# Performance work log

Measured on AMD Instinct MI355X. Metric: run time of the kernel, lower is better.

The kernel has to match this reference:

```python
import jax, jax.numpy as jnp
import numpy as np

NUM_HEADS = 8
HEAD_DIM = 64
HIDDEN_SIZE = 128
TOP_K = 16
EPS = 1e-6


def setup_inputs() -> dict:
    key = jax.random.key(0)
    k1, k2, k3 = jax.random.split(key, 3)
    B, H, S, D = 4, NUM_HEADS, 1024, HEAD_DIM
    return {
        "keys": jax.random.normal(k1, (B, H, S, D), dtype=jnp.float32),
        "values": jax.random.normal(k2, (B, H, S, D), dtype=jnp.float32),
        "queries": jax.random.normal(k3, (B, H, S, D), dtype=jnp.float32),
    }


def _project(x):
    # replicate [B,H,S,D] along last dim to cover HIDDEN_SIZE basis indices
    D = x.shape[-1]
    if D >= HIDDEN_SIZE:
        return x[..., :HIDDEN_SIZE]
    repeats = (HIDDEN_SIZE + D - 1) // D
    return jnp.tile(x, (1, 1, 1, repeats))[..., :HIDDEN_SIZE]


def reference(keys, values, queries):
    B, H, S, D = keys.shape
    b_idx = jnp.arange(B)[:, None, None]   # [B,1,1]
    h_idx = jnp.arange(H)[None, :, None]   # [1,H,1]

    # ---- update: scatter-add outer products into assigned memory bank ----
    assignments = jnp.argmax(jnp.abs(_project(keys)), axis=-1)  # [B,H,S]
    outer = values[..., :, None] * keys[..., None, :]           # [B,H,S,D,D] (v k^T)
    M = jnp.zeros((B, H, HIDDEN_SIZE, D, D), dtype=keys.dtype)
    M = M.at[b_idx, h_idx, assignments].add(outer)
    z = jnp.zeros((B, H, HIDDEN_SIZE, D), dtype=keys.dtype)
    z = z.at[b_idx, h_idx, assignments].add(keys)

    # ---- retrieve: top-k basis selection, gather-matvec, weighted combine ----
    scores = jnp.abs(_project(queries))                          # [B,H,S,HIDDEN]
    top_scores, top_idx = jax.lax.top_k(scores, TOP_K)           # [B,H,S,K]
    weights = jax.nn.softmax(top_scores, axis=-1)

    output = jnp.zeros((B, H, S, D), dtype=queries.dtype)
    for k in range(TOP_K):
        mem = top_idx[..., k]                                    # [B,H,S]
        M_sel = M[b_idx, h_idx, mem]                             # [B,H,S,D,D]
        z_sel = z[b_idx, h_idx, mem]                             # [B,H,S,D]
        num = jnp.einsum('bhsde,bhse->bhsd', M_sel, queries)
        den = jnp.einsum('bhsd,bhsd->bhs', z_sel, queries)[..., None] + EPS
        output = output + weights[..., k:k + 1] * (num / den)
    return output
```

## Files before the change

kernel.cpp:

```cpp
#include <hip/hip_runtime.h>
#include <math.h>

#define S_LEN 1024
#define EPS 1e-6f

typedef __attribute__((ext_vector_type(8)))  short bf16x8;
typedef __attribute__((ext_vector_type(4)))  short bf16x4;
typedef __attribute__((ext_vector_type(16))) float float16v;


__device__ __forceinline__ void bar_lgkm() {
    asm volatile("s_waitcnt lgkmcnt(0)" ::: "memory");
    __builtin_amdgcn_s_barrier();
    __builtin_amdgcn_sched_barrier(0);
    asm volatile("" ::: "memory");
}

__device__ __forceinline__ unsigned short f2bf(float f) {
    unsigned int u = __float_as_uint(f);
    unsigned int r = (u + 0x7fffu + ((u >> 16) & 1u)) >> 16;
    return (unsigned short)r;
}

__device__ __forceinline__ bf16x8 pack8(float4 a, float4 b) {
    bf16x8 r;
    r[0] = (short)f2bf(a.x); r[1] = (short)f2bf(a.y);
    r[2] = (short)f2bf(a.z); r[3] = (short)f2bf(a.w);
    r[4] = (short)f2bf(b.x); r[5] = (short)f2bf(b.y);
    r[6] = (short)f2bf(b.z); r[7] = (short)f2bf(b.w);
    return r;
}

__global__ __launch_bounds__(512) void k_pre(const float* __restrict__ keys,
                                             const float* __restrict__ queries,
                                             int* __restrict__ kcnt2,
                                             unsigned short* __restrict__ klist2,
                                             int* __restrict__ qcnt2,
                                             unsigned* __restrict__ qpair,
                                             unsigned char* __restrict__ qflag,
                                             float* __restrict__ out) {
    const int bh   = blockIdx.x >> 5;
    const int blk  = blockIdx.x & 31;
    const int wv   = threadIdx.x >> 6;
    const int lane = threadIdx.x & 63;

    __shared__ int khist[64], qhist[64];
    if (threadIdx.x < 64) { khist[threadIdx.x] = 0; qhist[threadIdx.x] = 0; }
    __syncthreads();

    const int s0 = blk * 32 + wv * 4;
    float kv[4], qv[4];
    #pragma unroll
    for (int i = 0; i < 4; ++i) {
        kv[i] = keys   [((size_t)bh * 1024 + s0 + i) * 64 + lane];
        qv[i] = queries[((size_t)bh * 1024 + s0 + i) * 64 + lane];
    }

    {
        float4 zz = {0.f, 0.f, 0.f, 0.f};
        float4* po = (float4*)(out + (size_t)blockIdx.x * 2048);
        po[threadIdx.x] = zz;
    }

    float bv[4]; int bi[4];
    #pragma unroll
    for (int i = 0; i < 4; ++i) { bv[i] = fabsf(kv[i]); bi[i] = lane; }
    #pragma unroll
    for (int off = 1; off < 64; off <<= 1) {
        #pragma unroll
        for (int i = 0; i < 4; ++i) {
            float ov = __shfl_xor(bv[i], off, 64);
            int   oi = __shfl_xor(bi[i], off, 64);
            if (ov > bv[i] || (ov == bv[i] && oi < bi[i])) { bv[i] = ov; bi[i] = oi; }
        }
    }
    #pragma unroll
    for (int i = 0; i < 4; ++i) {
        if (lane == 0) {
            int pos = atomicAdd(&khist[bi[i]], 1);
            klist2[((size_t)bh * 64 + bi[i]) * 1024 + blk * 32 + pos] =
                (unsigned short)(s0 + i);
        }
    }

    unsigned ud[4]; int gt[4];
    #pragma unroll
    for (int i = 0; i < 4; ++i) {
        ud[i] = __float_as_uint(qv[i]) & 0x7fffffffu;
        gt[i] = 0;
    }
    #pragma unroll
    for (int k = 0; k < 64; ++k) {
        #pragma unroll
        for (int i = 0; i < 4; ++i) {
            unsigned ui = (unsigned)__builtin_amdgcn_readlane((int)ud[i], k);
            gt[i] += (ui > ud[i]) ? 1 : 0;
        }
    }
    int S[4];
    #pragma unroll
    for (int i = 0; i < 4; ++i) S[i] = gt[i];
    #pragma unroll
    for (int off = 1; off < 64; off <<= 1) {
        #pragma unroll
        for (int i = 0; i < 4; ++i) S[i] += __shfl_xor(S[i], off, 64);
    }
    float e[4];
    #pragma unroll
    for (int i = 0; i < 4; ++i) e[i] = expf(__uint_as_float(ud[i]));
    int copies[4], contrib[4], rank[4];
    #pragma unroll
    for (int i = 0; i < 4; ++i) {
        if (S[i] == 2016) {
            contrib[i] = (gt[i] < 8);
            copies[i]  = contrib[i] ? 2 : 0;
            rank[i]    = gt[i];
        } else {
            int eq = 0, eql = 0;
            #pragma unroll
            for (int k = 0; k < 64; ++k) {
                unsigned ui = (unsigned)__builtin_amdgcn_readlane((int)ud[i], k);
                eq  += (ui == ud[i]) ? 1 : 0;
                eql += (ui == ud[i] && k < lane) ? 1 : 0;
            }
            int pos_low  = 2 * gt[i] + eql;
            int pos_high = pos_low + eq;
            copies[i]  = (pos_low < 16 ? 1 : 0) + (pos_high < 16 ? 1 : 0);
            contrib[i] = (pos_low < 16);
            rank[i]    = 15;
        }
    }
    float ce[4];
    #pragma unroll
    for (int i = 0; i < 4; ++i) ce[i] = (float)copies[i] * e[i];
    #pragma unroll
    for (int off = 1; off < 64; off <<= 1) {
        #pragma unroll
        for (int i = 0; i < 4; ++i) ce[i] += __shfl_xor(ce[i], off, 64);
    }
    #pragma unroll
    for (int i = 0; i < 4; ++i) {
        if (contrib[i]) {
            int pos = atomicAdd(&qhist[lane], 1);
            unsigned wb = __float_as_uint(e[i] / ce[i]) & 0xFFFFC000u;
            qpair[((size_t)bh * 64 + lane) * 1024 + blk * 32 + pos] =
                wb | ((unsigned)rank[i] << 10) | (unsigned)(s0 + i);
        }
        if (qflag && lane == 0)
            qflag[bh * 1024 + s0 + i] = (S[i] == 2016) ? 0 : 1;
    }
    __syncthreads();
    if (threadIdx.x < 64) {
        kcnt2[(bh * 32 + blk) * 64 + threadIdx.x] = khist[threadIdx.x];
        qcnt2[(bh * 32 + blk) * 64 + threadIdx.x] = qhist[threadIdx.x];
    }
}

__global__ __launch_bounds__(256) void k_build(const float* __restrict__ keys,
                                               const float* __restrict__ values,
                                               const int* __restrict__ kcnt2,
                                               const unsigned short* __restrict__ klist2,
                                               unsigned short* __restrict__ M_g,
                                               float* __restrict__ z_g,
                                               int* __restrict__ nm_g) {
    const int g    = blockIdx.x;
    const int bh   = g >> 6;
    const int bank = g & 63;
    const int t    = threadIdx.x;
    const int lane = t & 63;
    const int grp  = t >> 6;

    __shared__ float stg[2][1024];
    __shared__ unsigned short s_match[256];
    __shared__ int koffs_s[33];

    if (t < 32) {
        int c = kcnt2[(bh * 32 + t) * 64 + bank];
        #pragma unroll
        for (int off = 1; off < 32; off <<= 1) {
            int o = __shfl(c, t - off, 64);
            if (t >= off) c += o;
        }
        if (t == 0) koffs_s[0] = 0;
        koffs_s[t + 1] = c;
    }
    bar_lgkm();
    const int nm = koffs_s[32];
    if (t == 0) nm_g[g] = nm;
    if (nm == 0) return;

    float acc[16];
    #pragma unroll
    for (int m = 0; m < 16; ++m) acc[m] = 0.f;
    float zacc = 0.f;
    const float* kb = keys   + (size_t)bh * S_LEN * 64;
    const float* vb = values + (size_t)bh * S_LEN * 64;
    int it = 0;
    for (int cb = 0; cb < nm; cb += 256) {
        const int cn = min(256, nm - cb);
        bar_lgkm();
        if (t < cn) {
            int idx = cb + t;
            int seg = 0;
            #pragma unroll
            for (int i = 1; i < 32; ++i) if (idx >= koffs_s[i]) seg = i;
            s_match[t] = klist2[(size_t)(bh * 64 + bank) * 1024 + seg * 32 +
                                (idx - koffs_s[seg])];
        }
        bar_lgkm();
        for (int base = 0; base < cn; base += 8, ++it) {
            float* kst = stg[it & 1];
            float* vst = kst + 512;
            #pragma unroll
            for (int rr = 0; rr < 2; ++rr) {
                int row = grp + rr * 4;
                if (base + row < cn) {
                    int s = s_match[base + row];
                    kst[row * 64 + lane] = kb[(size_t)s * 64 + lane];
                    vst[row * 64 + lane] = vb[(size_t)s * 64 + lane];
                }
            }
            bar_lgkm();
            int lim = min(8, cn - base);
            for (int jj = 0; jj < lim; ++jj) {
                float kv = kst[jj * 64 + lane];
                #pragma unroll
                for (int m = 0; m < 16; ++m)
                    acc[m] += vst[jj * 64 + grp * 16 + m] * kv;
            }
            if (t < 64)
                for (int jj = 0; jj < lim; ++jj) zacc += kst[jj * 64 + t];
        }
    }
    unsigned short* mg = M_g + (size_t)g * 4096;
    #pragma unroll
    for (int m = 0; m < 16; ++m) {
        int dv = grp * 16 + m;
        mg[dv * 64 + (((lane >> 3) ^ (dv & 7)) << 3) + (lane & 7)] = f2bf(acc[m]);
    }
    if (t < 64) z_g[(size_t)g * 64 + t] = zacc;
}

template <bool GM, bool SC>
__global__ __launch_bounds__(256) void k_main_t(const float* __restrict__ keys,
                                                const float* __restrict__ values,
                                                const float* __restrict__ queries,
                                                const int* __restrict__ kcnt2,
                                                const unsigned short* __restrict__ klist2,
                                                const int* __restrict__ qcnt2,
                                                const unsigned* __restrict__ qpair,
                                                const unsigned short* __restrict__ M_g,
                                                const float* __restrict__ z_g,
                                                const int* __restrict__ nm_g,
                                                unsigned short* __restrict__ Obuf,
                                                float* __restrict__ out) {
    const int g     = blockIdx.x;
    const int gb    = g >> 1;
    const int split = g & 1;
    const int bh    = gb >> 6;
    const int bank  = gb & 63;
    const int t     = threadIdx.x;
    const int lane  = t & 63;
    const int grp   = t >> 6;

    __shared__ alignas(16) unsigned short M_bf[64 * 64];
    __shared__ alignas(16) unsigned short Q_bf[64 * 64];
    __shared__ alignas(16) unsigned short Ou_bf[64 * 68];
    __shared__ unsigned short s_match[256];
    __shared__ unsigned q_ent[256];
    __shared__ int    koffs_s[33], qoffs_s[33];
    __shared__ float  z_s[64];
    __shared__ double den_s[64];
    __shared__ float  w_s[2][64];
    __shared__ int    sq_s[2][64];

    if constexpr (GM) {
        if (t < 32) {
            int c = qcnt2[(bh * 32 + t) * 64 + bank];
            #pragma unroll
            for (int off = 1; off < 32; off <<= 1) {
                int o = __shfl(c, t - off, 64);
                if (t >= off) c += o;
            }
            if (t == 0) qoffs_s[0] = 0;
            qoffs_s[t + 1] = c;
        }
    } else {
        if (t < 64) {
            int i = t & 31;
            int c = (t < 32) ? kcnt2[(bh * 32 + i) * 64 + bank]
                             : qcnt2[(bh * 32 + i) * 64 + bank];
            #pragma unroll
            for (int off = 1; off < 32; off <<= 1) {
                int o = __shfl(c, t - off, 64);
                if (i >= off) c += o;
            }
            if (t < 32) { if (i == 0) koffs_s[0] = 0; koffs_s[i + 1] = c; }
            else        { if (i == 0) qoffs_s[0] = 0; qoffs_s[i + 1] = c; }
        }
    }
    bar_lgkm();

    const int nq   = qoffs_s[32];
    const int half = (nq + 1) >> 1;
    const int jlo  = split * half;
    const int jhi  = min(nq, jlo + half);
    int nm;
    if constexpr (GM) nm = nm_g[gb]; else nm = koffs_s[32];
    if (jhi <= jlo) return;
    if (nm == 0) {
        if constexpr (SC) {
            for (int jg = jlo + t; jg < jhi; jg += 256) {
                int seg = 0;
                #pragma unroll
                for (int i = 1; i < 32; ++i) if (jg >= qoffs_s[i]) seg = i;
                unsigned e = qpair[(size_t)(bh * 64 + bank) * 1024 + seg * 32 +
                                   (jg - qoffs_s[seg])];
                int r = (e >> 10) & 15;
                if (r < 8) {
                    uint4 z4 = {0u, 0u, 0u, 0u};
                    uint4* dst = (uint4*)&Obuf[(((size_t)bh * 1024 +
                                 (e & 1023u)) * 8 + r) * 64];
                    #pragma unroll
                    for (int x = 0; x < 8; ++x) dst[x] = z4;
                }
            }
        }
        return;
    }

    if constexpr (GM) {
        const unsigned short* mg = M_g + (size_t)gb * 4096;
        *(bf16x8*)&M_bf[t * 8]        = *(const bf16x8*)&mg[t * 8];
        *(bf16x8*)&M_bf[2048 + t * 8] = *(const bf16x8*)&mg[2048 + t * 8];
        if (t < 64) z_s[t] = z_g[(size_t)gb * 64 + t];
    } else {
        float acc[16];
        #pragma unroll
        for (int m = 0; m < 16; ++m) acc[m] = 0.f;
        float zacc = 0.f;
        const float* kb = keys   + (size_t)bh * S_LEN * 64;
        const float* vb = values + (size_t)bh * S_LEN * 64;
        int it = 0;
        for (int cb = 0; cb < nm; cb += 256) {
            const int cn = min(256, nm - cb);
            bar_lgkm();
            if (t < cn) {
                int idx = cb + t;
                int seg = 0;
                #pragma unroll
                for (int i = 1; i < 32; ++i) if (idx >= koffs_s[i]) seg = i;
                s_match[t] = klist2[(size_t)(bh * 64 + bank) * 1024 + seg * 32 +
                                    (idx - koffs_s[seg])];
            }
            bar_lgkm();
            for (int base = 0; base < cn; base += 8, ++it) {
                float* kst = (float*)Ou_bf + (it & 1) * 1024;
                float* vst = kst + 512;
                #pragma unroll
                for (int rr = 0; rr < 2; ++rr) {
                    int row = grp + rr * 4;
                    if (base + row < cn) {
                        int s = s_match[base + row];
                        kst[row * 64 + lane] = kb[(size_t)s * 64 + lane];
                        vst[row * 64 + lane] = vb[(size_t)s * 64 + lane];
                    }
                }
                bar_lgkm();
                int lim = min(8, cn - base);
                for (int jj = 0; jj < lim; ++jj) {
                    float kv = kst[jj * 64 + lane];
                    #pragma unroll
                    for (int m = 0; m < 16; ++m)
                        acc[m] += vst[jj * 64 + grp * 16 + m] * kv;
                }
                if (t < 64)
                    for (int jj = 0; jj < lim; ++jj) zacc += kst[jj * 64 + t];
            }
        }
        #pragma unroll
        for (int m = 0; m < 16; ++m) {
            int dv = grp * 16 + m;
            M_bf[dv * 64 + (((lane >> 3) ^ (dv & 7)) << 3) + (lane & 7)] = f2bf(acc[m]);
        }
        if (t < 64) z_s[t] = zacc;
    }

    const float* qb = queries + (size_t)bh * S_LEN * 64;
    float*       ob = out     + (size_t)bh * S_LEN * 64;
    unsigned short* obuf_b = SC ? Obuf + (size_t)bh * 1024 * 512 : nullptr;
    const int dvh = grp >> 1, jh = grp & 1;
    const int hi  = lane >> 5;
    const int nqL = jhi - jlo;
    const int jq  = t >> 2, cq = t & 3;

    int prev_nb = 0;
    bool have_pf = false;
    float4 f0, f1, f2, f3;
    unsigned pe = 0;
    for (int qloc = 0, batch = 0; qloc < nqL; qloc += 64, ++batch) {
        const int nb  = min(64, nqL - qloc);
        const int cur = batch & 1;

        if ((qloc & 255) == 0) {
            if (qloc + t < nqL) {
                int jg = jlo + qloc + t;
                int seg = 0;
                #pragma unroll
                for (int i = 1; i < 32; ++i) if (jg >= qoffs_s[i]) seg = i;
                q_ent[t] = qpair[(size_t)(bh * 64 + bank) * 1024 + seg * 32 +
                                 (jg - qoffs_s[seg])];
            }
            bar_lgkm();
        }

        unsigned e = 0;
        const bool act = (jq < nb);
        if (act) {
            e = have_pf ? pe : q_ent[(qloc & 255) + jq];
            if (!have_pf) {
                const float4* src =
                    (const float4*)(qb + (size_t)(e & 1023u) * 64 + cq * 16);
                f0 = src[0]; f1 = src[1]; f2 = src[2]; f3 = src[3];
            }
        }

        if (batch > 0) {
            #pragma unroll
            for (int jj = 0; jj < 16; ++jj) {
                int j = grp * 16 + jj;
                if (j < prev_nb) {
                    unsigned short vb16 = Ou_bf[j * 68 + lane];
                    int sr = sq_s[1 - cur][j];
                    int s  = sr & 1023;
                    if constexpr (SC) {
                        int r = (sr >> 10) & 15;
                        if (r < 8)
                            obuf_b[((size_t)s * 8 + r) * 64 + lane] = vb16;
                        else
                            unsafeAtomicAdd(&ob[(size_t)s * 64 + lane],
                                __uint_as_float((unsigned)vb16 << 16));
                    } else {
                        unsafeAtomicAdd(&ob[(size_t)s * 64 + lane],
                            __uint_as_float((unsigned)vb16 << 16));
                    }
                }
            }
        }

        {
            bf16x8 p0 = {}, p1 = {};
            double d = 0.0;
            if (act) {
                if ((t & 3) == 0) {
                    sq_s[cur][jq] = (int)(e & 0x3FFFu);
                    w_s[cur][jq]  = __uint_as_float(e & 0xFFFFC000u);
                }
                p0 = pack8(f0, f1);
                p1 = pack8(f2, f3);
                const float4* zz4 = (const float4*)&z_s[cq * 16];
                float4 z0 = zz4[0], z1 = zz4[1], z2 = zz4[2], z3 = zz4[3];
                double da, db;
                da  = (double)z0.x * f0.x + (double)z0.y * f0.y + (double)z0.z * f0.z + (double)z0.w * f0.w;
                db  = (double)z1.x * f1.x + (double)z1.y * f1.y + (double)z1.z * f1.z + (double)z1.w * f1.w;
                da += (double)z2.x * f2.x + (double)z2.y * f2.y + (double)z2.z * f2.z + (double)z2.w * f2.w;
                db += (double)z3.x * f3.x + (double)z3.y * f3.y + (double)z3.z * f3.z + (double)z3.w * f3.w;
                d = da + db;
            }
            int c0 = cq * 2;
            *(bf16x8*)&Q_bf[jq * 64 + ((c0 ^ (jq & 7)) << 3)]       = p0;
            *(bf16x8*)&Q_bf[jq * 64 + (((c0 + 1) ^ (jq & 7)) << 3)] = p1;
            d += __shfl_xor(d, 1, 64);
            d += __shfl_xor(d, 2, 64);
            if ((t & 3) == 0) den_s[jq] = d;
        }

        {
            const int qn = qloc + 64;
            have_pf = false;
            if (qn < nqL && (qn & 255) != 0) {
                int nbn = min(64, nqL - qn);
                if (jq < nbn) {
                    pe = q_ent[(qn & 255) + jq];
                    const float4* src =
                        (const float4*)(qb + (size_t)(pe & 1023u) * 64 + cq * 16);
                    f0 = src[0]; f1 = src[1]; f2 = src[2]; f3 = src[3];
                    have_pf = true;
                }
            }
        }
        bar_lgkm();

        float16v C;
        #pragma unroll
        for (int i = 0; i < 16; ++i) C[i] = 0.f;
        const int am = dvh * 32 + (lane & 31);
        const int bn = jh  * 32 + (lane & 31);
        #pragma unroll
        for (int ks = 0; ks < 4; ++ks) {
            int ch = ks * 2 + hi;
            bf16x8 af = *(const bf16x8*)&M_bf[am * 64 + ((ch ^ (am & 7)) << 3)];
            bf16x8 bf = *(const bf16x8*)&Q_bf[bn * 64 + ((ch ^ (bn & 7)) << 3)];
            C = __builtin_amdgcn_mfma_f32_32x32x16_bf16(af, bf, C, 0, 0, 0);
        }
        {
            double den = den_s[bn];
            float  w   = w_s[cur][bn];
            float rinv = (float)((double)w / (den + (double)EPS));
            #pragma unroll
            for (int rq = 0; rq < 4; ++rq) {
                bf16x4 pk;
                pk[0] = (short)f2bf(C[rq * 4 + 0] * rinv);
                pk[1] = (short)f2bf(C[rq * 4 + 1] * rinv);
                pk[2] = (short)f2bf(C[rq * 4 + 2] * rinv);
                pk[3] = (short)f2bf(C[rq * 4 + 3] * rinv);
                *(bf16x4*)&Ou_bf[bn * 68 + dvh * 32 + rq * 8 + hi * 4] = pk;
            }
        }
        bar_lgkm();
        prev_nb = nb;
    }
    {
        const int cur = (((nqL + 63) >> 6) - 1) & 1;
        #pragma unroll
        for (int jj = 0; jj < 16; ++jj) {
            int j = grp * 16 + jj;
            if (j < prev_nb) {
                unsigned short vb16 = Ou_bf[j * 68 + lane];
                int sr = sq_s[cur][j];
                int s  = sr & 1023;
                if constexpr (SC) {
                    int r = (sr >> 10) & 15;
                    if (r < 8)
                        obuf_b[((size_t)s * 8 + r) * 64 + lane] = vb16;
                    else
                        unsafeAtomicAdd(&ob[(size_t)s * 64 + lane],
                            __uint_as_float((unsigned)vb16 << 16));
                } else {
                    unsafeAtomicAdd(&ob[(size_t)s * 64 + lane],
                        __uint_as_float((unsigned)vb16 << 16));
                }
            }
        }
    }
}

__global__ __launch_bounds__(256) void k_reduce(const unsigned short* __restrict__ Obuf,
                                                const unsigned char* __restrict__ qflag,
                                                float* __restrict__ out) {
    const int wv   = threadIdx.x >> 6;
    const int lane = threadIdx.x & 63;
    const int q0   = (blockIdx.x * 4 + wv) * 8;
    #pragma unroll
    for (int i = 0; i < 8; ++i) {
        int q = q0 + i;
        if (qflag[q]) continue;
        const unsigned short* obr = Obuf + (size_t)q * 512;
        float acc = 0.f;
        #pragma unroll
        for (int r = 0; r < 8; ++r)
            acc += __uint_as_float((unsigned)obr[r * 64 + lane] << 16);
        out[(size_t)q * 64 + lane] = acc;
    }
}

extern "C" void kernel_launch(void* const* d_in, const int* in_sizes, int n_in,
                              void* d_out, int out_size, void* d_ws, size_t ws_size,
                              hipStream_t stream) {
    const float* keys    = (const float*)d_in[0];
    const float* values  = (const float*)d_in[1];
    const float* queries = (const float*)d_in[2];
    char* ws = (char*)d_ws;
    int*            kcnt2  = (int*)(ws);
    int*            qcnt2  = (int*)(ws + 262144);
    unsigned short* klist2 = (unsigned short*)(ws + 524288);
    unsigned*       qpair  = (unsigned*)(ws + 4718592);
    unsigned short* M_g    = (unsigned short*)(ws + 13107200);
    float*          z_g    = (float*)(ws + 29884416);
    int*            nm_g   = (int*)(ws + 30408704);
    unsigned char*  qflag  = (unsigned char*)(ws + 30416896);
    unsigned short* Obuf   = (unsigned short*)(ws + 30449664);
    const bool big  = (ws_size >= 30416896u);
    const bool big2 = (ws_size >= 64004096u);

    k_pre<<<1024, 512, 0, stream>>>(keys, queries, kcnt2, klist2, qcnt2, qpair,
                                    big2 ? qflag : nullptr, (float*)d_out);
    if (big2) {
        k_build<<<2048, 256, 0, stream>>>(keys, values, kcnt2, klist2,
                                          M_g, z_g, nm_g);
        k_main_t<true, true><<<4096, 256, 0, stream>>>(keys, values, queries,
            kcnt2, klist2, qcnt2, qpair, M_g, z_g, nm_g, Obuf, (float*)d_out);
        k_reduce<<<1024, 256, 0, stream>>>(Obuf, qflag, (float*)d_out);
    } else if (big) {
        k_build<<<2048, 256, 0, stream>>>(keys, values, kcnt2, klist2,
                                          M_g, z_g, nm_g);
        k_main_t<true, false><<<4096, 256, 0, stream>>>(keys, values, queries,
            kcnt2, klist2, qcnt2, qpair, M_g, z_g, nm_g, Obuf, (float*)d_out);
    } else {
        k_main_t<false, false><<<4096, 256, 0, stream>>>(keys, values, queries,
            kcnt2, klist2, qcnt2, qpair, M_g, z_g, nm_g, Obuf, (float*)d_out);
    }
}
```

Measured before the change: 144.0 us.

## Fuse memory-bank build into main kernel and use LDS for query rank counting

Removes the separate k_build kernel and the global M/z staging buffers, so each main-kernel block builds its own bank matrix in registers/LDS and processes all of that bank's queries, with no two-way split. This drops one launch and a global round-trip of M. The cost is that the bank-build work no longer runs in its own kernel and the grid halves to 2048 blocks, which lowers parallelism for banks with many queries. Separately, k_pre replaces the 64 readlane comparisons per row with vectorized uint4 reads of staged magnitudes from LDS.

Result: faster. 132.9 us (-7.7%).

```diff
diff --git a/kernel.cpp b/kernel.cpp
--- a/kernel.cpp
+++ b/kernel.cpp
@@ -15,6 +15,8 @@
     __builtin_amdgcn_sched_barrier(0);
     asm volatile("" ::: "memory");
 }
+
+#define PIN(x) asm volatile("" : "+v"(x))
 
 __device__ __forceinline__ unsigned short f2bf(float f) {
     unsigned int u = __float_as_uint(f);
@@ -45,6 +47,7 @@
     const int lane = threadIdx.x & 63;
 
     __shared__ int khist[64], qhist[64];
+    __shared__ alignas(16) unsigned rq_s[8][4][64];
     if (threadIdx.x < 64) { khist[threadIdx.x] = 0; qhist[threadIdx.x] = 0; }
     __syncthreads();
 
@@ -60,6 +63,16 @@
         float4 zz = {0.f, 0.f, 0.f, 0.f};
         float4* po = (float4*)(out + (size_t)blockIdx.x * 2048);
         po[threadIdx.x] = zz;
+    }
+
+    #pragma unroll
+    for (int i = 0; i < 4; ++i) { PIN(kv[i]); PIN(qv[i]); }
+
+    unsigned ud[4];
+    #pragma unroll
+    for (int i = 0; i < 4; ++i) {
+        ud[i] = __float_as_uint(qv[i]) & 0x7fffffffu;
+        rq_s[wv][i][lane] = ud[i];
     }
 
     float bv[4]; int bi[4];
@@ -83,18 +96,16 @@
         }
     }
 
-    unsigned ud[4]; int gt[4];
-    #pragma unroll
-    for (int i = 0; i < 4; ++i) {
-        ud[i] = __float_as_uint(qv[i]) & 0x7fffffffu;
-        gt[i] = 0;
-    }
-    #pragma unroll
-    for (int k = 0; k < 64; ++k) {
+    int gt[4] = {0, 0, 0, 0};
+    #pragma unroll
+    for (int k4 = 0; k4 < 16; ++k4) {
         #pragma unroll
         for (int i = 0; i < 4; ++i) {
-            unsigned ui = (unsigned)__builtin_amdgcn_readlane((int)ud[i], k);
-            gt[i] += (ui > ud[i]) ? 1 : 0;
+            const uint4 vv = *(const uint4*)&rq_s[wv][i][k4 * 4];
+            gt[i] += (vv.x > ud[i]) ? 1 : 0;
+            gt[i] += (vv.y > ud[i]) ? 1 : 0;
+            gt[i] += (vv.z > ud[i]) ? 1 : 0;
+            gt[i] += (vv.w > ud[i]) ? 1 : 0;
         }
     }
     int S[4];
@@ -156,109 +167,19 @@
     }
 }
 
-__global__ __launch_bounds__(256) void k_build(const float* __restrict__ keys,
+template <bool SC>
+__global__ __launch_bounds__(256) void k_mainB(const float* __restrict__ keys,
                                                const float* __restrict__ values,
+                                               const float* __restrict__ queries,
                                                const int* __restrict__ kcnt2,
                                                const unsigned short* __restrict__ klist2,
-                                               unsigned short* __restrict__ M_g,
-                                               float* __restrict__ z_g,
-                                               int* __restrict__ nm_g) {
-    const int g    = blockIdx.x;
-    const int bh   = g >> 6;
-    const int bank = g & 63;
-    const int t    = threadIdx.x;
-    const int lane = t & 63;
-    const int grp  = t >> 6;
-
-    __shared__ float stg[2][1024];
-    __shared__ unsigned short s_match[256];
-    __shared__ int koffs_s[33];
-
-    if (t < 32) {
-        int c = kcnt2[(bh * 32 + t) * 64 + bank];
-        #pragma unroll
-        for (int off = 1; off < 32; off <<= 1) {
-            int o = __shfl(c, t - off, 64);
-            if (t >= off) c += o;
-        }
-        if (t == 0) koffs_s[0] = 0;
-        koffs_s[t + 1] = c;
-    }
-    bar_lgkm();
-    const int nm = koffs_s[32];
-    if (t == 0) nm_g[g] = nm;
-    if (nm == 0) return;
-
-    float acc[16];
-    #pragma unroll
-    for (int m = 0; m < 16; ++m) acc[m] = 0.f;
-    float zacc = 0.f;
-    const float* kb = keys   + (size_t)bh * S_LEN * 64;
-    const float* vb = values + (size_t)bh * S_LEN * 64;
-    int it = 0;
-    for (int cb = 0; cb < nm; cb += 256) {
-        const int cn = min(256, nm - cb);
-        bar_lgkm();
-        if (t < cn) {
-            int idx = cb + t;
-            int seg = 0;
-            #pragma unroll
-            for (int i = 1; i < 32; ++i) if (idx >= koffs_s[i]) seg = i;
-            s_match[t] = klist2[(size_t)(bh * 64 + bank) * 1024 + seg * 32 +
-                                (idx - koffs_s[seg])];
-        }
-        bar_lgkm();
-        for (int base = 0; base < cn; base += 8, ++it) {
-            float* kst = stg[it & 1];
-            float* vst = kst + 512;
-            #pragma unroll
-            for (int rr = 0; rr < 2; ++rr) {
-                int row = grp + rr * 4;
-                if (base + row < cn) {
-                    int s = s_match[base + row];
-                    kst[row * 64 + lane] = kb[(size_t)s * 64 + lane];
-                    vst[row * 64 + lane] = vb[(size_t)s * 64 + lane];
-                }
-            }
-            bar_lgkm();
-            int lim = min(8, cn - base);
-            for (int jj = 0; jj < lim; ++jj) {
-                float kv = kst[jj * 64 + lane];
-                #pragma unroll
-                for (int m = 0; m < 16; ++m)
-                    acc[m] += vst[jj * 64 + grp * 16 + m] * kv;
-            }
-            if (t < 64)
-                for (int jj = 0; jj < lim; ++jj) zacc += kst[jj * 64 + t];
-        }
-    }
-    unsigned short* mg = M_g + (size_t)g * 4096;
-    #pragma unroll
-    for (int m = 0; m < 16; ++m) {
-        int dv = grp * 16 + m;
-        mg[dv * 64 + (((lane >> 3) ^ (dv & 7)) << 3) + (lane & 7)] = f2bf(acc[m]);
-    }
-    if (t < 64) z_g[(size_t)g * 64 + t] = zacc;
-}
-
-template <bool GM, bool SC>
-__global__ __launch_bounds__(256) void k_main_t(const float* __restrict__ keys,
-                                                const float* __restrict__ values,
-                                                const float* __restrict__ queries,
-                                                const int* __restrict__ kcnt2,
-                                                const unsigned short* __restrict__ klist2,
-                                                const int* __restrict__ qcnt2,
-                                                const unsigned* __restrict__ qpair,
-                                                const unsigned short* __restrict__ M_g,
-                                                const float* __restrict__ z_g,
-                                                const int* __restrict__ nm_g,
-                                                unsigned short* __restrict__ Obuf,
-                                                float* __restrict__ out) {
+                                               const int* __restrict__ qcnt2,
+                                               const unsigned* __restrict__ qpair,
+                                               unsigned short* __restrict__ Obuf,
+                                               float* __restrict__ out) {
     const int g     = blockIdx.x;
-    const int gb    = g >> 1;
-    const int split = g & 1;
-    const int bh    = gb >> 6;
-    const int bank  = gb & 63;
+    const int bh    = g >> 6;
+    const int bank  = g & 63;
     const int t     = threadIdx.x;
     const int lane  = t & 63;
     const int grp   = t >> 6;
@@ -274,43 +195,26 @@
     __shared__ float  w_s[2][64];
     __shared__ int    sq_s[2][64];
 
-    if constexpr (GM) {
-        if (t < 32) {
-            int c = qcnt2[(bh * 32 + t) * 64 + bank];
-            #pragma unroll
-            for (int off = 1; off < 32; off <<= 1) {
-                int o = __shfl(c, t - off, 64);
-                if (t >= off) c += o;
-            }
-            if (t == 0) qoffs_s[0] = 0;
-            qoffs_s[t + 1] = c;
-        }
-    } else {
-        if (t < 64) {
-            int i = t & 31;
-            int c = (t < 32) ? kcnt2[(bh * 32 + i) * 64 + bank]
-                             : qcnt2[(bh * 32 + i) * 64 + bank];
-            #pragma unroll
-            for (int off = 1; off < 32; off <<= 1) {
-                int o = __shfl(c, t - off, 64);
-                if (i >= off) c += o;
-            }
-            if (t < 32) { if (i == 0) koffs_s[0] = 0; koffs_s[i + 1] = c; }
-            else        { if (i == 0) qoffs_s[0] = 0; qoffs_s[i + 1] = c; }
-        }
+    if (t < 64) {
+        int i = t & 31;
+        int c = (t < 32) ? kcnt2[(bh * 32 + i) * 64 + bank]
+                         : qcnt2[(bh * 32 + i) * 64 + bank];
+        #pragma unroll
+        for (int off = 1; off < 32; off <<= 1) {
+            int o = __shfl(c, t - off, 64);
+            if (i >= off) c += o;
+        }
+        if (t < 32) { if (i == 0) koffs_s[0] = 0; koffs_s[i + 1] = c; }
+        else        { if (i == 0) qoffs_s[0] = 0; qoffs_s[i + 1] = c; }
     }
     bar_lgkm();
 
-    const int nq   = qoffs_s[32];
-    const int half = (nq + 1) >> 1;
-    const int jlo  = split * half;
-    const int jhi  = min(nq, jlo + half);
-    int nm;
-    if constexpr (GM) nm = nm_g[gb]; else nm = koffs_s[32];
-    if (jhi <= jlo) return;
+    const int nq = qoffs_s[32];
+    const int nm = koffs_s[32];
+    if (nq == 0) return;
     if (nm == 0) {
         if constexpr (SC) {
-            for (int jg = jlo + t; jg < jhi; jg += 256) {
+            for (int jg = t; jg < nq; jg += 256) {
                 int seg = 0;
                 #pragma unroll
                 for (int i = 1; i < 32; ++i) if (jg >= qoffs_s[i]) seg = i;
@@ -329,12 +233,7 @@
         return;
     }
 
-    if constexpr (GM) {
-        const unsigned short* mg = M_g + (size_t)gb * 4096;
-        *(bf16x8*)&M_bf[t * 8]        = *(const bf16x8*)&mg[t * 8];
-        *(bf16x8*)&M_bf[2048 + t * 8] = *(const bf16x8*)&mg[2048 + t * 8];
-        if (t < 64) z_s[t] = z_g[(size_t)gb * 64 + t];
-    } else {
+    {
         float acc[16];
         #pragma unroll
         for (int m = 0; m < 16; ++m) acc[m] = 0.f;
@@ -391,20 +290,19 @@
     unsigned short* obuf_b = SC ? Obuf + (size_t)bh * 1024 * 512 : nullptr;
     const int dvh = grp >> 1, jh = grp & 1;
     const int hi  = lane >> 5;
-    const int nqL = jhi - jlo;
     const int jq  = t >> 2, cq = t & 3;
 
     int prev_nb = 0;
     bool have_pf = false;
     float4 f0, f1, f2, f3;
     unsigned pe = 0;
-    for (int qloc = 0, batch = 0; qloc < nqL; qloc += 64, ++batch) {
-        const int nb  = min(64, nqL - qloc);
+    for (int qloc = 0, batch = 0; qloc < nq; qloc += 64, ++batch) {
+        const int nb  = min(64, nq - qloc);
         const int cur = batch & 1;
 
         if ((qloc & 255) == 0) {
-            if (qloc + t < nqL) {
-                int jg = jlo + qloc + t;
+            if (qloc + t < nq) {
+                int jg = qloc + t;
                 int seg = 0;
                 #pragma unroll
                 for (int i = 1; i < 32; ++i) if (jg >= qoffs_s[i]) seg = i;
@@ -478,8 +376,8 @@
         {
             const int qn = qloc + 64;
             have_pf = false;
-            if (qn < nqL && (qn & 255) != 0) {
-                int nbn = min(64, nqL - qn);
+            if (qn < nq && (qn & 255) != 0) {
+                int nbn = min(64, nq - qn);
                 if (jq < nbn) {
                     pe = q_ent[(qn & 255) + jq];
                     const float4* src =
@@ -521,7 +419,7 @@
         prev_nb = nb;
     }
     {
-        const int cur = (((nqL + 63) >> 6) - 1) & 1;
+        const int cur = (((nq + 63) >> 6) - 1) & 1;
         #pragma unroll
         for (int jj = 0; jj < 16; ++jj) {
             int j = grp * 16 + jj;
@@ -575,29 +473,20 @@
     int*            qcnt2  = (int*)(ws + 262144);
     unsigned short* klist2 = (unsigned short*)(ws + 524288);
     unsigned*       qpair  = (unsigned*)(ws + 4718592);
-    unsigned short* M_g    = (unsigned short*)(ws + 13107200);
-    float*          z_g    = (float*)(ws + 29884416);
-    int*            nm_g   = (int*)(ws + 30408704);
     unsigned char*  qflag  = (unsigned char*)(ws + 30416896);
     unsigned short* Obuf   = (unsigned short*)(ws + 30449664);
-    const bool big  = (ws_size >= 30416896u);
     const bool big2 = (ws_size >= 64004096u);
 
     k_pre<<<1024, 512, 0, stream>>>(keys, queries, kcnt2, klist2, qcnt2, qpair,
                                     big2 ? qflag : nullptr, (float*)d_out);
     if (big2) {
-        k_build<<<2048, 256, 0, stream>>>(keys, values, kcnt2, klist2,
-                                          M_g, z_g, nm_g);
-        k_main_t<true, true><<<4096, 256, 0, stream>>>(keys, values, queries,
-            kcnt2, klist2, qcnt2, qpair, M_g, z_g, nm_g, Obuf, (float*)d_out);
+        k_mainB<true><<<2048, 256, 0, stream>>>(keys, values, queries, kcnt2,
+                                                klist2, qcnt2, qpair, Obuf,
+                                                (float*)d_out);
         k_reduce<<<1024, 256, 0, stream>>>(Obuf, qflag, (float*)d_out);
-    } else if (big) {
-        k_build<<<2048, 256, 0, stream>>>(keys, values, kcnt2, klist2,
-                                          M_g, z_g, nm_g);
-        k_main_t<true, false><<<4096, 256, 0, stream>>>(keys, values, queries,
-            kcnt2, klist2, qcnt2, qpair, M_g, z_g, nm_g, Obuf, (float*)d_out);
     } else {
-        k_main_t<false, false><<<4096, 256, 0, stream>>>(keys, values, queries,
-            kcnt2, klist2, qcnt2, qpair, M_g, z_g, nm_g, Obuf, (float*)d_out);
-    }
-}
+        k_mainB<false><<<2048, 256, 0, stream>>>(keys, values, queries, kcnt2,
+                                                 klist2, qcnt2, qpair, Obuf,
+                                                 (float*)d_out);
+    }
+}
```
